# Optimization experiments

Measured on AMD Instinct MI355X. Metric: run time of the kernel, lower is better.

The kernel has to match this reference:

```python
import jax, jax.numpy as jnp
import numpy as np

_NUM_RBF = 8
_R_MAX = 3.0  # randn point clouds have radius ~ sqrt(3)
_CENTERS = jnp.linspace(0.0, _R_MAX, _NUM_RBF)
_C15 = float(np.sqrt(15.0))
_C5 = float(np.sqrt(5.0))


def _sph_basis(positions):
    """map_3d_feats_to_basis_functions: 8x0e (radial RBFs) + 1x1o (l=1 SH) + 1x2e (l=2 SH)."""
    centered = positions - jnp.mean(positions, axis=-2, keepdims=True)  # [B,N,3]
    r = jnp.sqrt(jnp.sum(centered * centered, axis=-1) + 1e-12)         # [B,N]
    d = centered / r[..., None]                                         # unit directions
    x, y, z = d[..., 0], d[..., 1], d[..., 2]
    s0 = jnp.exp(-(r[..., None] - _CENTERS) ** 2)                       # [B,N,8] scalar feats (0e)
    sh1 = d                                                             # [B,N,3] (1o)
    sh2 = jnp.stack([_C15 * x * y,
                     _C15 * y * z,
                     0.5 * _C5 * (3.0 * z * z - 1.0),
                     _C15 * x * z,
                     0.5 * _C15 * (x * x - y * y)], axis=-1)            # [B,N,5] (2e)
    return s0, sh1, sh2


def _mix(feat, W):
    # Equivariant per-l channel mixing: feat [B, mul_in, dim_l], W [mul_in, mul_out]
    return jnp.einsum('bci,co->boi', feat, W) / jnp.sqrt(jnp.asarray(W.shape[0], feat.dtype))


def reference(positions, W1a, W1b, W1c, W1d, W2a, W2b, W2c):
    s0, sh1, sh2 = _sph_basis(positions)
    # avg_irreps_with_same_id: average over the N points axis
    s = jnp.mean(s0, axis=-2)[..., None]          # [B,8,1]  8x0e
    v = jnp.mean(sh1, axis=-2)[:, None, :]        # [B,1,3]  1x1o
    # (mean of sh2 is dropped: linear1 output has no 2e)
    # linear1: '8x0e+1x1o+1x2e' -> '6x0e+4x1o' -> '6x0e+4x1o'
    s = _mix(_mix(s, W1a), W1b)                   # [B,6,1]
    v = _mix(_mix(v, W1c), W1d)                   # [B,4,3]
    # linear2: '6x0e+4x1o' -> '6x0e+4x1o' -> '6x0e'
    s = _mix(_mix(s, W2a), W2b)                   # [B,6,1]
    _ = _mix(v, W2c)                              # mid 1o channel, dropped by '6x0e' output
    # torch.cat of the six 0e irreps -> [B,6]
    return s[..., 0]


def setup_inputs() -> dict:
    key = jax.random.key(0)
    ks = jax.random.split(key, 8)
    return {
        'positions': jax.random.normal(ks[0], (32768, 128, 3), dtype=jnp.float32),
        'W1a': jax.random.normal(ks[1], (8, 6), dtype=jnp.float32),
        'W1b': jax.random.normal(ks[2], (6, 6), dtype=jnp.float32),
        'W1c': jax.random.normal(ks[3], (1, 4), dtype=jnp.float32),
        'W1d': jax.random.normal(ks[4], (4, 4), dtype=jnp.float32),
        'W2a': jax.random.normal(ks[5], (6, 6), dtype=jnp.float32),
        'W2b': jax.random.normal(ks[6], (6, 6), dtype=jnp.float32),
        'W2c': jax.random.normal(ks[7], (4, 4), dtype=jnp.float32),
    }
```

## Files before the change

### kernel.cpp

```cpp
#include <hip/hip_runtime.h>


template <int N>
__device__ __forceinline__ float ror16(float v) {
    return __int_as_float(__builtin_amdgcn_update_dpp(
        0, __float_as_int(v), 0x120 | N, 0xF, 0xF, true));
}
__device__ __forceinline__ float rowsum16(float v) {
    v += ror16<1>(v);
    v += ror16<2>(v);
    v += ror16<4>(v);
    v += ror16<8>(v);
    return v;
}

__global__ __launch_bounds__(256, 8) void sph_fused(
    const float* __restrict__ pos,
    const float* __restrict__ W1a, const float* __restrict__ W1b,
    const float* __restrict__ W2a, const float* __restrict__ W2b,
    float* __restrict__ out, int nBatch)
{
    __shared__ float BBs[36];
    __shared__ float CCs[36];
    __shared__ float MMs[48];

    const int t = threadIdx.x;

    if (t < 36) {
        const int c = t / 6, o = t - 6 * c;
        float s = 0.f;
        #pragma unroll
        for (int j = 0; j < 6; ++j) s += W2a[c * 6 + j] * W2b[j * 6 + o];
        BBs[t] = s;
    }
    __syncthreads();
    if (t < 36) {
        const int c = t / 6, o = t - 6 * c;
        float s = 0.f;
        #pragma unroll
        for (int j = 0; j < 6; ++j) s += W1b[c * 6 + j] * BBs[j * 6 + o];
        CCs[t] = s;
    }
    __syncthreads();
    if (t < 48) {
        const int k = t / 6, o = t - 6 * k;
        float s = 0.f;
        #pragma unroll
        for (int c = 0; c < 6; ++c) s += W1a[k * 6 + c] * CCs[c * 6 + o];
        const float WKtab[8] = {1.0f, 0.83220583f, 0.47965235f, 0.19146295f,
                                0.05293049f, 0.01013418f, 0.00134381f, 1.2340980e-4f};
        MMs[t] = s * WKtab[k] * (0.024056261216234408f / 128.0f);
    }
    __syncthreads();

    const int lane = t & 63;
    const int w    = t >> 6;
    const int lsub = lane & 15;
    const int grp  = lane >> 4;

    const int nTiles = (nBatch + 3) >> 2;
    const int tile = blockIdx.x * 4 + w;
    if (tile >= nTiles) return;

    const float4* __restrict__ p4 = reinterpret_cast<const float4*>(pos);
    int base = tile * 384 + grp * 96 + lsub * 6;
    const int maxC = nBatch * 96 - 6;
    if (base > maxC) base = maxC;

    union { float4 q[6]; float f[24]; } u;
    #pragma unroll
    for (int j = 0; j < 6; ++j) u.q[j] = p4[base + j];

    float sx = 0.f, sy = 0.f, sz = 0.f;
    #pragma unroll
    for (int i = 0; i < 8; ++i) {
        sx += u.f[3 * i + 0]; sy += u.f[3 * i + 1]; sz += u.f[3 * i + 2];
    }
    sx = rowsum16(sx); sy = rowsum16(sy); sz = rowsum16(sz);
    const float mx = sx * (1.f / 128.f), my = sy * (1.f / 128.f), mz = sz * (1.f / 128.f);

    float a0 = 0.f, a1 = 0.f, a2 = 0.f, a3 = 0.f,
          a4 = 0.f, a5 = 0.f, a6 = 0.f, a7 = 0.f;
    #pragma unroll
    for (int i = 0; i < 8; ++i) {
        const float dx = u.f[3 * i + 0] - mx;
        const float dy = u.f[3 * i + 1] - my;
        const float dz = u.f[3 * i + 2] - mz;
        const float r2 = fmaf(dx, dx, fmaf(dy, dy, fmaf(dz, dz, 1e-12f)));
        float r;
        asm("v_sqrt_f32 %0, %1" : "=v"(r) : "v"(r2));
        const float E0 = __expf(-r2);
        const float Bf = __expf(r * (6.0f / 7.0f));
        float p = E0;
        a0 += E0;
        p *= Bf; a1 += p;
        p *= Bf; a2 += p;
        p *= Bf; a3 += p;
        p *= Bf; a4 += p;
        p *= Bf; a5 += p;
        p *= Bf; a6 += p;
        p *= Bf; a7 += p;
    }
    a0 = rowsum16(a0); a1 = rowsum16(a1); a2 = rowsum16(a2); a3 = rowsum16(a3);
    a4 = rowsum16(a4); a5 = rowsum16(a5); a6 = rowsum16(a6); a7 = rowsum16(a7);

    const int col = (lsub < 6) ? lsub : 0;
    float o_ = a0 * MMs[0 * 6 + col];
    o_ = fmaf(a1, MMs[1 * 6 + col], o_);
    o_ = fmaf(a2, MMs[2 * 6 + col], o_);
    o_ = fmaf(a3, MMs[3 * 6 + col], o_);
    o_ = fmaf(a4, MMs[4 * 6 + col], o_);
    o_ = fmaf(a5, MMs[5 * 6 + col], o_);
    o_ = fmaf(a6, MMs[6 * 6 + col], o_);
    o_ = fmaf(a7, MMs[7 * 6 + col], o_);

    const int batch = tile * 4 + grp;
    if (lsub < 6 && batch < nBatch) out[batch * 6 + lsub] = o_;
}

extern "C" void kernel_launch(void* const* d_in, const int* in_sizes, int n_in,
                              void* d_out, int out_size, void* d_ws, size_t ws_size,
                              hipStream_t stream) {
    const float* pos = (const float*)d_in[0];
    const float* W1a = (const float*)d_in[1];
    const float* W1b = (const float*)d_in[2];
    const float* W2a = (const float*)d_in[5];
    const float* W2b = (const float*)d_in[6];
    float* out = (float*)d_out;

    const int nBatch = in_sizes[0] / 384;
    const int nTiles = (nBatch + 3) / 4;
    const int grid = (nTiles + 3) / 4;

    sph_fused<<<dim3(grid), dim3(256), 0, stream>>>(pos, W1a, W1b, W2a, W2b, out, nBatch);
}
```

Measured before the change: 14.96 us.

## Stage coalesced position loads through LDS and halve batches per wave

Each wave now handles two batches instead of four. Every lane covers 4 points instead of 8, and the cross-lane reduction gains a ds_swizzle xor-16 step to combine two 16-lane rows. Positions are loaded with fully coalesced per-lane float4 reads into a per-wave LDS staging buffer, then redistributed so each lane gets its own 12 floats. This replaces strided multi-float4 loads per lane and doubles the grid. The cost is 12 KB of LDS per block, an LDS round trip, and extra shuffle work per batch.

New measurement: 16.23 us. 1.08x slower.

```diff
diff --git a/kernel.cpp b/kernel.cpp
--- a/kernel.cpp
+++ b/kernel.cpp
@@ -13,6 +13,9 @@
     v += ror16<8>(v);
     return v;
 }
+__device__ __forceinline__ float xor16_add(float v) {
+    return v + __int_as_float(__builtin_amdgcn_ds_swizzle(__float_as_int(v), 0x401F));
+}
 
 __global__ __launch_bounds__(256, 8) void sph_fused(
     const float* __restrict__ pos,
@@ -23,6 +26,7 @@
     __shared__ float BBs[36];
     __shared__ float CCs[36];
     __shared__ float MMs[48];
+    __shared__ float4 stage[4][192];
 
     const int t = threadIdx.x;
 
@@ -55,34 +59,37 @@
 
     const int lane = t & 63;
     const int w    = t >> 6;
-    const int lsub = lane & 15;
-    const int grp  = lane >> 4;
 
-    const int nTiles = (nBatch + 3) >> 2;
+    const int nTiles = (nBatch + 1) >> 1;
     const int tile = blockIdx.x * 4 + w;
     if (tile >= nTiles) return;
 
     const float4* __restrict__ p4 = reinterpret_cast<const float4*>(pos);
-    int base = tile * 384 + grp * 96 + lsub * 6;
-    const int maxC = nBatch * 96 - 6;
-    if (base > maxC) base = maxC;
+    const int lastC = nBatch * 96 - 1;
+    #pragma unroll
+    for (int j = 0; j < 3; ++j) {
+        int gc = tile * 192 + 64 * j + lane;
+        if (gc > lastC) gc = lastC;
+        stage[w][64 * j + lane] = p4[gc];
+    }
+    asm volatile("s_waitcnt lgkmcnt(0)" ::: "memory");
 
-    union { float4 q[6]; float f[24]; } u;
+    union { float4 q[3]; float f[12]; } u;
     #pragma unroll
-    for (int j = 0; j < 6; ++j) u.q[j] = p4[base + j];
+    for (int s = 0; s < 3; ++s) u.q[s] = stage[w][3 * lane + s];
 
-    float sx = 0.f, sy = 0.f, sz = 0.f;
-    #pragma unroll
-    for (int i = 0; i < 8; ++i) {
-        sx += u.f[3 * i + 0]; sy += u.f[3 * i + 1]; sz += u.f[3 * i + 2];
-    }
-    sx = rowsum16(sx); sy = rowsum16(sy); sz = rowsum16(sz);
+    float sx = u.f[0] + u.f[3] + u.f[6] + u.f[9];
+    float sy = u.f[1] + u.f[4] + u.f[7] + u.f[10];
+    float sz = u.f[2] + u.f[5] + u.f[8] + u.f[11];
+    sx = xor16_add(rowsum16(sx));
+    sy = xor16_add(rowsum16(sy));
+    sz = xor16_add(rowsum16(sz));
     const float mx = sx * (1.f / 128.f), my = sy * (1.f / 128.f), mz = sz * (1.f / 128.f);
 
     float a0 = 0.f, a1 = 0.f, a2 = 0.f, a3 = 0.f,
           a4 = 0.f, a5 = 0.f, a6 = 0.f, a7 = 0.f;
     #pragma unroll
-    for (int i = 0; i < 8; ++i) {
+    for (int i = 0; i < 4; ++i) {
         const float dx = u.f[3 * i + 0] - mx;
         const float dy = u.f[3 * i + 1] - my;
         const float dz = u.f[3 * i + 2] - mz;
@@ -101,10 +108,13 @@
         p *= Bf; a6 += p;
         p *= Bf; a7 += p;
     }
-    a0 = rowsum16(a0); a1 = rowsum16(a1); a2 = rowsum16(a2); a3 = rowsum16(a3);
-    a4 = rowsum16(a4); a5 = rowsum16(a5); a6 = rowsum16(a6); a7 = rowsum16(a7);
+    a0 = xor16_add(rowsum16(a0)); a1 = xor16_add(rowsum16(a1));
+    a2 = xor16_add(rowsum16(a2)); a3 = xor16_add(rowsum16(a3));
+    a4 = xor16_add(rowsum16(a4)); a5 = xor16_add(rowsum16(a5));
+    a6 = xor16_add(rowsum16(a6)); a7 = xor16_add(rowsum16(a7));
 
-    const int col = (lsub < 6) ? lsub : 0;
+    const int idx = lane & 31;
+    const int col = (idx < 6) ? idx : 0;
     float o_ = a0 * MMs[0 * 6 + col];
     o_ = fmaf(a1, MMs[1 * 6 + col], o_);
     o_ = fmaf(a2, MMs[2 * 6 + col], o_);
@@ -114,8 +124,8 @@
     o_ = fmaf(a6, MMs[6 * 6 + col], o_);
     o_ = fmaf(a7, MMs[7 * 6 + col], o_);
 
-    const int batch = tile * 4 + grp;
-    if (lsub < 6 && batch < nBatch) out[batch * 6 + lsub] = o_;
+    const int batch = tile * 2 + (lane >> 5);
+    if (idx < 6 && batch < nBatch) out[batch * 6 + idx] = o_;
 }
 
 extern "C" void kernel_launch(void* const* d_in, const int* in_sizes, int n_in,
@@ -129,7 +139,7 @@
     float* out = (float*)d_out;
 
     const int nBatch = in_sizes[0] / 384;
-    const int nTiles = (nBatch + 3) / 4;
+    const int nTiles = (nBatch + 1) / 2;
     const int grid = (nTiles + 3) / 4;
 
     sph_fused<<<dim3(grid), dim3(256), 0, stream>>>(pos, W1a, W1b, W2a, W2b, out, nBatch);
```

## Load points with coalesced 12-byte per-lane reads and transpose-reduce RBF sums

Applied to the files above, without the earlier changes.

Each lane now loads one xyz point per step, so a wave reads 64 consecutive points at a time and the access is coalesced, replacing the earlier 96-byte per-lane float4 runs. The kernel processes the wave's 4 batches one after another. Per batch it reduces the centroid across the full wave and folds the 8 RBF accumulators with a transpose-style butterfly shuffle, so lane k ends up holding channel k. The final mixing uses readlane broadcasts, and outputs are written as 24 contiguous floats per tile. The aim is better memory coalescing and fewer reduction ops, at the cost of more cross-lane shuffles and serialized per-batch reductions.

New measurement: 16.33 us. 1.09x slower.

```diff
diff --git a/kernel.cpp b/kernel.cpp
--- a/kernel.cpp
+++ b/kernel.cpp
@@ -1,17 +1,32 @@
 #include <hip/hip_runtime.h>
 
 
-template <int N>
-__device__ __forceinline__ float ror16(float v) {
+struct __attribute__((packed, aligned(4))) F3 { float x, y, z; };
+
+template <int C>
+__device__ __forceinline__ float dppmov(float v) {
     return __int_as_float(__builtin_amdgcn_update_dpp(
-        0, __float_as_int(v), 0x120 | N, 0xF, 0xF, true));
+        0, __float_as_int(v), C, 0xF, 0xF, true));
+}
+template <int PAT>
+__device__ __forceinline__ float swzf(float v) {
+    return __int_as_float(__builtin_amdgcn_ds_swizzle(__float_as_int(v), PAT));
 }
 __device__ __forceinline__ float rowsum16(float v) {
-    v += ror16<1>(v);
-    v += ror16<2>(v);
-    v += ror16<4>(v);
-    v += ror16<8>(v);
+    v += dppmov<0x121>(v);
+    v += dppmov<0x122>(v);
+    v += dppmov<0x124>(v);
+    v += dppmov<0x128>(v);
     return v;
+}
+__device__ __forceinline__ float wsum64(float v) {
+    v = rowsum16(v);
+    v += swzf<0x401F>(v);
+    v += __shfl_xor(v, 32, 64);
+    return v;
+}
+__device__ __forceinline__ float rlane(float v, int k) {
+    return __int_as_float(__builtin_amdgcn_readlane(__float_as_int(v), k));
 }
 
 __global__ __launch_bounds__(256, 8) void sph_fused(
@@ -55,67 +70,104 @@
 
     const int lane = t & 63;
     const int w    = t >> 6;
-    const int lsub = lane & 15;
-    const int grp  = lane >> 4;
 
     const int nTiles = (nBatch + 3) >> 2;
     const int tile = blockIdx.x * 4 + w;
     if (tile >= nTiles) return;
 
-    const float4* __restrict__ p4 = reinterpret_cast<const float4*>(pos);
-    int base = tile * 384 + grp * 96 + lsub * 6;
-    const int maxC = nBatch * 96 - 6;
-    if (base > maxC) base = maxC;
+    const int qsel = lane / 6;
+    const int col  = (lane < 24) ? (lane - 6 * qsel) : 0;
+    float Mc[8];
+    #pragma unroll
+    for (int k = 0; k < 8; ++k) Mc[k] = MMs[k * 6 + col];
 
-    union { float4 q[6]; float f[24]; } u;
+    const int maxPt = nBatch * 128 - 1;
+    float px[8], py[8], pz[8];
     #pragma unroll
-    for (int j = 0; j < 6; ++j) u.q[j] = p4[base + j];
+    for (int s = 0; s < 8; ++s) {
+        int pt = tile * 512 + s * 64 + lane;
+        if (pt > maxPt) pt = maxPt;
+        const F3 v = *reinterpret_cast<const F3*>(pos + 3 * (size_t)pt);
+        px[s] = v.x; py[s] = v.y; pz[s] = v.z;
+    }
 
-    float sx = 0.f, sy = 0.f, sz = 0.f;
+    float ov = 0.f;
+
     #pragma unroll
-    for (int i = 0; i < 8; ++i) {
-        sx += u.f[3 * i + 0]; sy += u.f[3 * i + 1]; sz += u.f[3 * i + 2];
+    for (int q = 0; q < 4; ++q) {
+        const int k0 = 2 * q, k1 = 2 * q + 1;
+
+        const float mx = wsum64(px[k0] + px[k1]) * (1.f / 128.f);
+        const float my = wsum64(py[k0] + py[k1]) * (1.f / 128.f);
+        const float mz = wsum64(pz[k0] + pz[k1]) * (1.f / 128.f);
+
+        float a0 = 0.f, a1 = 0.f, a2 = 0.f, a3 = 0.f,
+              a4 = 0.f, a5 = 0.f, a6 = 0.f, a7 = 0.f;
+        #pragma unroll
+        for (int h = 0; h < 2; ++h) {
+            const int s = 2 * q + h;
+            const float dx = px[s] - mx;
+            const float dy = py[s] - my;
+            const float dz = pz[s] - mz;
+            const float r2 = fmaf(dx, dx, fmaf(dy, dy, fmaf(dz, dz, 1e-12f)));
+            float r;
+            asm("v_sqrt_f32 %0, %1" : "=v"(r) : "v"(r2));
+            const float E0 = __expf(-r2);
+            const float Bf = __expf(r * (6.0f / 7.0f));
+            float p = E0;
+            a0 += E0;
+            p *= Bf; a1 += p;
+            p *= Bf; a2 += p;
+            p *= Bf; a3 += p;
+            p *= Bf; a4 += p;
+            p *= Bf; a5 += p;
+            p *= Bf; a6 += p;
+            p *= Bf; a7 += p;
+        }
+
+        const int l0 = lane & 1, l1 = (lane >> 1) & 1, l2 = (lane >> 2) & 1;
+        float b0, b1, b2, b3;
+        {
+            const float s0 = l0 ? a0 : a1, k0_ = l0 ? a1 : a0;
+            const float s1 = l0 ? a2 : a3, k1_ = l0 ? a3 : a2;
+            const float s2 = l0 ? a4 : a5, k2_ = l0 ? a5 : a4;
+            const float s3 = l0 ? a6 : a7, k3_ = l0 ? a7 : a6;
+            b0 = k0_ + __shfl_xor(s0, 1, 64);
+            b1 = k1_ + __shfl_xor(s1, 1, 64);
+            b2 = k2_ + __shfl_xor(s2, 1, 64);
+            b3 = k3_ + __shfl_xor(s3, 1, 64);
+        }
+        float c0, c1;
+        {
+            const float s0 = l1 ? b0 : b1, k0_ = l1 ? b1 : b0;
+            const float s1 = l1 ? b2 : b3, k1_ = l1 ? b3 : b2;
+            c0 = k0_ + __shfl_xor(s0, 2, 64);
+            c1 = k1_ + __shfl_xor(s1, 2, 64);
+        }
+        float S;
+        {
+            const float s0 = l2 ? c0 : c1, k0_ = l2 ? c1 : c0;
+            S = k0_ + __shfl_xor(s0, 4, 64);
+        }
+        S += __shfl_xor(S, 8, 64);
+        S += __shfl_xor(S, 16, 64);
+        S += __shfl_xor(S, 32, 64);
+
+        float o_ = rlane(S, 0) * Mc[0];
+        o_ = fmaf(rlane(S, 1), Mc[1], o_);
+        o_ = fmaf(rlane(S, 2), Mc[2], o_);
+        o_ = fmaf(rlane(S, 3), Mc[3], o_);
+        o_ = fmaf(rlane(S, 4), Mc[4], o_);
+        o_ = fmaf(rlane(S, 5), Mc[5], o_);
+        o_ = fmaf(rlane(S, 6), Mc[6], o_);
+        o_ = fmaf(rlane(S, 7), Mc[7], o_);
+
+        ov = (qsel == q) ? o_ : ov;
     }
-    sx = rowsum16(sx); sy = rowsum16(sy); sz = rowsum16(sz);
-    const float mx = sx * (1.f / 128.f), my = sy * (1.f / 128.f), mz = sz * (1.f / 128.f);
 
-    float a0 = 0.f, a1 = 0.f, a2 = 0.f, a3 = 0.f,
-          a4 = 0.f, a5 = 0.f, a6 = 0.f, a7 = 0.f;
-    #pragma unroll
-    for (int i = 0; i < 8; ++i) {
-        const float dx = u.f[3 * i + 0] - mx;
-        const float dy = u.f[3 * i + 1] - my;
-        const float dz = u.f[3 * i + 2] - mz;
-        const float r2 = fmaf(dx, dx, fmaf(dy, dy, fmaf(dz, dz, 1e-12f)));
-        float r;
-        asm("v_sqrt_f32 %0, %1" : "=v"(r) : "v"(r2));
-        const float E0 = __expf(-r2);
-        const float Bf = __expf(r * (6.0f / 7.0f));
-        float p = E0;
-        a0 += E0;
-        p *= Bf; a1 += p;
-        p *= Bf; a2 += p;
-        p *= Bf; a3 += p;
-        p *= Bf; a4 += p;
-        p *= Bf; a5 += p;
-        p *= Bf; a6 += p;
-        p *= Bf; a7 += p;
-    }
-    a0 = rowsum16(a0); a1 = rowsum16(a1); a2 = rowsum16(a2); a3 = rowsum16(a3);
-    a4 = rowsum16(a4); a5 = rowsum16(a5); a6 = rowsum16(a6); a7 = rowsum16(a7);
-
-    const int col = (lsub < 6) ? lsub : 0;
-    float o_ = a0 * MMs[0 * 6 + col];
-    o_ = fmaf(a1, MMs[1 * 6 + col], o_);
-    o_ = fmaf(a2, MMs[2 * 6 + col], o_);
-    o_ = fmaf(a3, MMs[3 * 6 + col], o_);
-    o_ = fmaf(a4, MMs[4 * 6 + col], o_);
-    o_ = fmaf(a5, MMs[5 * 6 + col], o_);
-    o_ = fmaf(a6, MMs[6 * 6 + col], o_);
-    o_ = fmaf(a7, MMs[7 * 6 + col], o_);
-
-    const int batch = tile * 4 + grp;
-    if (lsub < 6 && batch < nBatch) out[batch * 6 + lsub] = o_;
+    const int batch = tile * 4 + qsel;
+    if (lane < 24 && batch < nBatch)
+        out[(size_t)tile * 24 + lane] = ov;
 }
 
 extern "C" void kernel_launch(void* const* d_in, const int* in_sizes, int n_in,
```
